# Kernel tuning notes

Measured on AMD Instinct MI355X. Metric: run time of the kernel, lower is better.

Reference implementation:

```python
import jax, jax.numpy as jnp
import numpy as np

SAMPLE = 16          # init kwarg `sample`
DILATED_RATE = 2     # init kwarg `dilated_rate`
RADIUS = 16.0        # hardcoded in forward: ball_query(16, ...)
NSAMPLE = SAMPLE * DILATED_RATE
XYZ_SCALE = 30.0     # spread points so radius-16 ball is a real neighborhood


def setup_inputs() -> dict:
    key = jax.random.key(0)
    k1, k2 = jax.random.split(key)
    xyz = jax.random.normal(k1, (4, 4096, 3), dtype=jnp.float32) * XYZ_SCALE
    feature = jax.random.normal(k2, (4, 4096, 64), dtype=jnp.float32)
    return {"xyz": xyz, "feature": feature}


def _ball_query(xyz, radius, nsample):
    """pointnet2-style ball query: for each point, the first `nsample` point
    indices (in ascending index order) with squared distance < radius^2;
    rows with fewer than nsample hits are padded with the first hit.
    xyz: [B,N,3] -> idx int32 [B,N,nsample]."""
    B, N, _ = xyz.shape
    sq = jnp.sum(xyz * xyz, axis=-1)                                   # [B,N]
    d2 = sq[:, :, None] + sq[:, None, :] - 2.0 * jnp.einsum(
        'bnd,bmd->bnm', xyz, xyz)                                      # [B,N,N]
    in_ball = d2 < (radius * radius)
    # score = N - j for in-ball points, 0 otherwise; top_k then returns the
    # smallest in-ball indices j, already sorted ascending in j.
    col_score = (N - jnp.arange(N, dtype=jnp.int32))[None, None, :]
    score = jnp.where(in_ball, col_score, 0)                           # [B,N,N]
    vals, idx = jax.lax.top_k(score, nsample)                          # [B,N,K]
    first = idx[..., 0:1]
    return jnp.where(vals > 0, idx, first)                             # pad with first hit


def _group(points, idx):
    """grouping_operation: points [B,N,C] (channel-last), idx [B,N,K] ->
    grouped [B,C,N,K]."""
    gathered = jax.vmap(lambda p, i: p[i])(points, idx)  # [B,N,K,C]
    return gathered.transpose(0, 3, 1, 2)                # [B,C,N,K]


def reference(xyz, feature):
    ids = _ball_query(xyz, RADIUS, NSAMPLE)              # [B,N,NSAMPLE]
    center = ids[:, :, 0:1]
    if DILATED_RATE == 1:
        dilated_ids = ids[:, :, :SAMPLE]
    else:
        region = ids[:, :, (DILATED_RATE - 1) * SAMPLE: DILATED_RATE * SAMPLE - 1]
        dilated_ids = jnp.concatenate([center, region], axis=-1)  # [B,N,SAMPLE]
    dilated_xyz = _group(xyz, dilated_ids)          # [B,3,N,SAMPLE]
    dilated_feature = _group(feature, dilated_ids)  # [B,C,N,SAMPLE]
    return (dilated_xyz, dilated_feature)
```

## Files before the change

### kernel.cpp

```cpp
#include <hip/hip_runtime.h>


#define BB 4
#define NN 4096
#define KK 16
#define PLANE (NN * KK)
#define NC 20
#define NCELLS (NC * NC * NC)

__device__ __forceinline__ int cell1d(float v)
{
    int c = (int)floorf((v + 160.0f) * 0.0625f);
    c = c < 0 ? 0 : c;
    return c > (NC - 1) ? (NC - 1) : c;
}

__global__ __launch_bounds__(256)
void preprocess(const float* __restrict__ xyz, float4* __restrict__ P,
                float4* __restrict__ SP, int* __restrict__ CS)
{
#pragma clang fp contract(off)
    __shared__ int hist[NCELLS];
    __shared__ int wsum[4];

    const int b = blockIdx.x;
    const int t = threadIdx.x;
    const int lane = t & 63, wave = t >> 6;
    const float* xb = xyz + b * NN * 3;

    for (int c = t; c < NCELLS; c += 256) hist[c] = 0;
    __syncthreads();

    for (int i = t; i < NN; i += 256) {
        const float x = xb[3 * i], y = xb[3 * i + 1], z = xb[3 * i + 2];
        const float sq = (x * x + y * y) + z * z;
        P[(b << 12) + i] = make_float4(x, y, z, sq);
        const int c = (cell1d(z) * NC + cell1d(y)) * NC + cell1d(x);
        atomicAdd(&hist[c], 1);
    }
    __syncthreads();

    const int c0 = t * 32;
    const int c1 = (c0 + 32 < NCELLS) ? c0 + 32 : NCELLS;
    int s = 0;
    for (int c = c0; c < c1; ++c) s += hist[c];
    int x = s;
#pragma unroll
    for (int off = 1; off < 64; off <<= 1) {
        const int u = __shfl_up(x, off, 64);
        if (lane >= off) x += u;
    }
    if (lane == 63) wsum[wave] = x;
    __syncthreads();
    int wb = 0;
    for (int w = 0; w < wave; ++w) wb += wsum[w];
    int acc = wb + x - s;

    int* cs = CS + b * (NCELLS + 1);
    for (int c = c0; c < c1; ++c) {
        const int v = hist[c];
        cs[c]   = acc;
        hist[c] = acc;
        acc += v;
    }
    if (t == 0) cs[NCELLS] = NN;
    __syncthreads();

    for (int i = t; i < NN; i += 256) {
        const float x = xb[3 * i], y = xb[3 * i + 1], z = xb[3 * i + 2];
        const int c = (cell1d(z) * NC + cell1d(y)) * NC + cell1d(x);
        const int slot = atomicAdd(&hist[c], 1);
        SP[(b << 12) + slot] = make_float4(x, y, z, __int_as_float(i));
    }
}

__global__ __launch_bounds__(256, 4)
void query_gather(const float4* __restrict__ P, const float4* __restrict__ SP,
                  const int* __restrict__ CS, const float* __restrict__ feat,
                  float* __restrict__ out)
{
#pragma clang fp contract(off)
    __shared__ unsigned int mask[4][128];
    __shared__ int sids[4 * KK];

    const int beta = blockIdx.x;
    const int b    = beta >> 10;
    const int p0   = (beta & 1023) * 4;
    const int t    = threadIdx.x;
    const int lane = t & 63;
    const int wave = t >> 6;

    ((unsigned int*)mask)[t]       = 0u;
    ((unsigned int*)mask)[t + 256] = 0u;
    __syncthreads();

    const float4* Pb  = P  + (b << 12);
    const float4* Sb  = SP + (b << 12);
    const int*    csb = CS + b * (NCELLS + 1);

    const float4 pi = Pb[p0 + wave];

    {
        const float sqi = pi.w;
        unsigned int* m = mask[wave];
        const int cx = cell1d(pi.x), cy = cell1d(pi.y), cz = cell1d(pi.z);
        const int xlo = cx > 0 ? cx - 1 : 0;
        const int xhi = cx < NC - 1 ? cx + 1 : NC - 1;

        int ss[9], se[9];
#pragma unroll
        for (int dz = 0; dz < 3; ++dz)
#pragma unroll
            for (int dy = 0; dy < 3; ++dy) {
                int zz = cz + dz - 1; zz = zz < 0 ? 0 : (zz > NC - 1 ? NC - 1 : zz);
                int yy = cy + dy - 1; yy = yy < 0 ? 0 : (yy > NC - 1 ? NC - 1 : yy);
                const int cb = (zz * NC + yy) * NC;
                ss[dz * 3 + dy] = csb[cb + xlo];
                se[dz * 3 + dy] = csb[cb + xhi + 1];
            }

        int off[10], base[9];
        off[0] = 0;
#pragma unroll
        for (int i = 0; i < 9; ++i) {
            off[i + 1] = off[i] + (se[i] - ss[i]);
            base[i]    = ss[i] - off[i];
        }
        const int T = off[9];

        for (int u = lane; u < T; u += 64) {
            int bsel = base[0];
#pragma unroll
            for (int i = 1; i < 9; ++i) bsel = (u >= off[i]) ? base[i] : bsel;
            const float4 a = Sb[u + bsel];
            const float sqj = (a.x * a.x + a.y * a.y) + a.z * a.z;
            const float dot = (pi.x * a.x + pi.y * a.y) + pi.z * a.z;
            const float d2  = (sqi + sqj) - 2.0f * dot;
            if (d2 < 256.0f) {
                const int j = __float_as_int(a.w);
                atomicOr(&m[j >> 5], 1u << (j & 31));
            }
        }
    }
    __syncthreads();

    {
        const unsigned int* m = mask[wave];
        const unsigned int lo  = m[2 * lane];
        const unsigned int hiw = m[2 * lane + 1];
        const unsigned long long w = ((unsigned long long)hiw << 32) | lo;
        const int c = __popcll(w);
        int x = c;
#pragma unroll
        for (int off = 1; off < 64; off <<= 1) {
            const int u = __shfl_up(x, off, 64);
            if (lane >= off) x += u;
        }
        const int cnt  = __shfl(x, 63, 64);
        const int base = x - c;

        int fj = 0x7fffffff;
        if (w) fj = (lane << 6) + __builtin_ctzll(w);
        for (int off = 32; off; off >>= 1) {
            const int o = __shfl_xor(fj, off, 64);
            fj = fj < o ? fj : o;
        }

        int* row = sids + wave * KK;
        if (w && base <= 30 && base + c > 16) {
            unsigned long long ww = w;
            int r = base;
            while (ww) {
                if (r > 30) break;
                if (r >= 16) row[r - 15] = (lane << 6) + __builtin_ctzll(ww);
                ww &= ww - 1;
                ++r;
            }
        }
        const int hi = (cnt < 31 ? cnt : 31) - 16;
        if (lane < KK && (lane == 0 || lane > hi)) row[lane] = fj;
    }
    __syncthreads();

    const int rowi = t & 63;
    const int part = t >> 6;
    const int id   = sids[rowi];
    const int ob   = (beta & 1023) * 64 + rowi;

    if (part == 0) {
        const float4 p = Pb[id];
        float* o0 = out + (size_t)b * 3 * PLANE + ob;
        o0[0]         = p.x;
        o0[PLANE]     = p.y;
        o0[2 * PLANE] = p.z;
    }

    const float4* frow = reinterpret_cast<const float4*>(feat + ((size_t)(b << 12) + id) * 64) + part * 4;
    float* o1 = out + (size_t)BB * 3 * PLANE + (size_t)b * 64 * PLANE
                    + (size_t)(part * 16) * PLANE + ob;
#pragma unroll
    for (int q = 0; q < 4; ++q) {
        const float4 v = frow[q];
        float* oc = o1 + (size_t)(4 * q) * PLANE;
        oc[0]         = v.x;
        oc[PLANE]     = v.y;
        oc[2 * PLANE] = v.z;
        oc[3 * PLANE] = v.w;
    }
}

extern "C" void kernel_launch(void* const* d_in, const int* in_sizes, int n_in,
                              void* d_out, int out_size, void* d_ws, size_t ws_size,
                              hipStream_t stream) {
    const float* xyz  = (const float*)d_in[0];
    const float* feat = (const float*)d_in[1];
    float* out = (float*)d_out;

    char* ws = (char*)d_ws;
    float4* P         = (float4*)(ws);
    float4* SP        = (float4*)(ws + 262144);
    int*    CS        = (int*)   (ws + 524288);

    preprocess  <<<BB,           256, 0, stream>>>(xyz, P, SP, CS);
    query_gather<<<BB * NN / 4,  256, 0, stream>>>(P, SP, CS, feat, out);
}
```

Before: 115.4 us.

## Process queries in cell-sorted order, prefetch candidates, and pad histogram to cut conflicts

Each block now takes its four query points from the cell-sorted array rather than in original index order. Neighbouring blocks therefore scan overlapping cells, which should improve cache reuse of candidate points. The output offset is recovered from the stored original index. The candidate loop is software-pipelined so the next chunk's load is issued before the current chunk's distance test. Each wave clears and uses its own mask, which lets the block-wide barriers around the scan be dropped. The preprocess histogram is padded every 32 entries to reduce LDS bank conflicts. The risks are scattered output writes, since consecutive blocks no longer write contiguous rows, and reliance on wave-level ordering of LDS operations now that the barriers are gone.

```diff
diff --git a/kernel.cpp b/kernel.cpp
--- a/kernel.cpp
+++ b/kernel.cpp
@@ -7,6 +7,7 @@
 #define PLANE (NN * KK)
 #define NC 20
 #define NCELLS (NC * NC * NC)
+#define HP(c) ((c) + ((c) >> 5))
 
 __device__ __forceinline__ int cell1d(float v)
 {
@@ -20,7 +21,7 @@
                 float4* __restrict__ SP, int* __restrict__ CS)
 {
 #pragma clang fp contract(off)
-    __shared__ int hist[NCELLS];
+    __shared__ int hist[HP(NCELLS - 1) + 1 + 8];
     __shared__ int wsum[4];
 
     const int b = blockIdx.x;
@@ -28,7 +29,7 @@
     const int lane = t & 63, wave = t >> 6;
     const float* xb = xyz + b * NN * 3;
 
-    for (int c = t; c < NCELLS; c += 256) hist[c] = 0;
+    for (int c = t; c < NCELLS; c += 256) hist[HP(c)] = 0;
     __syncthreads();
 
     for (int i = t; i < NN; i += 256) {
@@ -36,14 +37,14 @@
         const float sq = (x * x + y * y) + z * z;
         P[(b << 12) + i] = make_float4(x, y, z, sq);
         const int c = (cell1d(z) * NC + cell1d(y)) * NC + cell1d(x);
-        atomicAdd(&hist[c], 1);
+        atomicAdd(&hist[HP(c)], 1);
     }
     __syncthreads();
 
     const int c0 = t * 32;
     const int c1 = (c0 + 32 < NCELLS) ? c0 + 32 : NCELLS;
     int s = 0;
-    for (int c = c0; c < c1; ++c) s += hist[c];
+    for (int c = c0; c < c1; ++c) s += hist[HP(c)];
     int x = s;
 #pragma unroll
     for (int off = 1; off < 64; off <<= 1) {
@@ -58,9 +59,9 @@
 
     int* cs = CS + b * (NCELLS + 1);
     for (int c = c0; c < c1; ++c) {
-        const int v = hist[c];
-        cs[c]   = acc;
-        hist[c] = acc;
+        const int v = hist[HP(c)];
+        cs[c]      = acc;
+        hist[HP(c)] = acc;
         acc += v;
     }
     if (t == 0) cs[NCELLS] = NN;
@@ -69,7 +70,7 @@
     for (int i = t; i < NN; i += 256) {
         const float x = xb[3 * i], y = xb[3 * i + 1], z = xb[3 * i + 2];
         const int c = (cell1d(z) * NC + cell1d(y)) * NC + cell1d(x);
-        const int slot = atomicAdd(&hist[c], 1);
+        const int slot = atomicAdd(&hist[HP(c)], 1);
         SP[(b << 12) + slot] = make_float4(x, y, z, __int_as_float(i));
     }
 }
@@ -82,28 +83,29 @@
 #pragma clang fp contract(off)
     __shared__ unsigned int mask[4][128];
     __shared__ int sids[4 * KK];
+    __shared__ int jof[4];
 
     const int beta = blockIdx.x;
     const int b    = beta >> 10;
-    const int p0   = (beta & 1023) * 4;
+    const int q0   = (beta & 1023) * 4;
     const int t    = threadIdx.x;
     const int lane = t & 63;
     const int wave = t >> 6;
 
-    ((unsigned int*)mask)[t]       = 0u;
-    ((unsigned int*)mask)[t + 256] = 0u;
-    __syncthreads();
-
     const float4* Pb  = P  + (b << 12);
     const float4* Sb  = SP + (b << 12);
     const int*    csb = CS + b * (NCELLS + 1);
 
-    const float4 pi = Pb[p0 + wave];
+    const float4 pr  = Sb[q0 + wave];
+    const float  sqi = (pr.x * pr.x + pr.y * pr.y) + pr.z * pr.z;
+    if (lane == 0) jof[wave] = __float_as_int(pr.w);
+
+    unsigned int* m = mask[wave];
+    m[2 * lane]     = 0u;
+    m[2 * lane + 1] = 0u;
 
     {
-        const float sqi = pi.w;
-        unsigned int* m = mask[wave];
-        const int cx = cell1d(pi.x), cy = cell1d(pi.y), cz = cell1d(pi.z);
+        const int cx = cell1d(pr.x), cy = cell1d(pr.y), cz = cell1d(pr.z);
         const int xlo = cx > 0 ? cx - 1 : 0;
         const int xhi = cx < NC - 1 ? cx + 1 : NC - 1;
 
@@ -128,24 +130,33 @@
         }
         const int T = off[9];
 
-        for (int u = lane; u < T; u += 64) {
-            int bsel = base[0];
-#pragma unroll
-            for (int i = 1; i < 9; ++i) bsel = (u >= off[i]) ? base[i] : bsel;
-            const float4 a = Sb[u + bsel];
+        auto sbaddr = [&](int u) {
+            int bs = base[0];
+#pragma unroll
+            for (int i = 1; i < 9; ++i) bs = (u >= off[i]) ? base[i] : bs;
+            return u + bs;
+        };
+
+        const int nch = (T + 63) >> 6;
+        float4 a = Sb[sbaddr(lane < T ? lane : T - 1)];
+        for (int c = 0; c < nch; ++c) {
+            float4 nx;
+            if (c + 1 < nch) {
+                const int un0 = lane + ((c + 1) << 6);
+                nx = Sb[sbaddr(un0 < T ? un0 : T - 1)];
+            }
             const float sqj = (a.x * a.x + a.y * a.y) + a.z * a.z;
-            const float dot = (pi.x * a.x + pi.y * a.y) + pi.z * a.z;
+            const float dot = (pr.x * a.x + pr.y * a.y) + pr.z * a.z;
             const float d2  = (sqi + sqj) - 2.0f * dot;
             if (d2 < 256.0f) {
                 const int j = __float_as_int(a.w);
                 atomicOr(&m[j >> 5], 1u << (j & 31));
             }
-        }
-    }
-    __syncthreads();
+            a = nx;
+        }
+    }
 
     {
-        const unsigned int* m = mask[wave];
         const unsigned int lo  = m[2 * lane];
         const unsigned int hiw = m[2 * lane + 1];
         const unsigned long long w = ((unsigned long long)hiw << 32) | lo;
@@ -185,7 +196,7 @@
     const int rowi = t & 63;
     const int part = t >> 6;
     const int id   = sids[rowi];
-    const int ob   = (beta & 1023) * 64 + rowi;
+    const int ob   = jof[rowi >> 4] * KK + (rowi & 15);
 
     if (part == 0) {
         const float4 p = Pb[id];
@@ -217,10 +228,10 @@
     float* out = (float*)d_out;
 
     char* ws = (char*)d_ws;
-    float4* P         = (float4*)(ws);
-    float4* SP        = (float4*)(ws + 262144);
-    int*    CS        = (int*)   (ws + 524288);
-
-    preprocess  <<<BB,           256, 0, stream>>>(xyz, P, SP, CS);
-    query_gather<<<BB * NN / 4,  256, 0, stream>>>(P, SP, CS, feat, out);
-}
+    float4* P  = (float4*)(ws);
+    float4* SP = (float4*)(ws + 262144);
+    int*    CS = (int*)   (ws + 524288);
+
+    preprocess  <<<BB,          256, 0, stream>>>(xyz, P, SP, CS);
+    query_gather<<<BB * NN / 4, 256, 0, stream>>>(P, SP, CS, feat, out);
+}
```

New measurement: 125.2 us. +8.5%, slower.

## Switch 3D cell grid to 2D xy columns and drop block-wide syncs

Applied to the files above, without the earlier changes.

The spatial grid now bins points only by x and y (20x20 columns) instead of a 20x20x20 voxel grid. The query therefore scans three contiguous column ranges, which removes the per-candidate 9-way segment selection. The per-wave mask is now cleared by its own wave, so the two __syncthreads around the candidate scan are dropped and only a wave-local dependency remains. The trade is more candidates per query, since the full z extent is scanned. Correctness also relies on wave-level LDS ordering without an explicit barrier.

```diff
diff --git a/kernel.cpp b/kernel.cpp
--- a/kernel.cpp
+++ b/kernel.cpp
@@ -6,7 +6,7 @@
 #define KK 16
 #define PLANE (NN * KK)
 #define NC 20
-#define NCELLS (NC * NC * NC)
+#define NCELL2 (NC * NC)
 
 __device__ __forceinline__ int cell1d(float v)
 {
@@ -20,7 +20,7 @@
                 float4* __restrict__ SP, int* __restrict__ CS)
 {
 #pragma clang fp contract(off)
-    __shared__ int hist[NCELLS];
+    __shared__ int hist[NCELL2];
     __shared__ int wsum[4];
 
     const int b = blockIdx.x;
@@ -28,20 +28,21 @@
     const int lane = t & 63, wave = t >> 6;
     const float* xb = xyz + b * NN * 3;
 
-    for (int c = t; c < NCELLS; c += 256) hist[c] = 0;
+    if (t < NCELL2) hist[t] = 0;
+    if (t + 256 < NCELL2) hist[t + 256] = 0;
     __syncthreads();
 
     for (int i = t; i < NN; i += 256) {
         const float x = xb[3 * i], y = xb[3 * i + 1], z = xb[3 * i + 2];
         const float sq = (x * x + y * y) + z * z;
         P[(b << 12) + i] = make_float4(x, y, z, sq);
-        const int c = (cell1d(z) * NC + cell1d(y)) * NC + cell1d(x);
+        const int c = cell1d(y) * NC + cell1d(x);
         atomicAdd(&hist[c], 1);
     }
     __syncthreads();
 
-    const int c0 = t * 32;
-    const int c1 = (c0 + 32 < NCELLS) ? c0 + 32 : NCELLS;
+    const int c0 = t * 2;
+    const int c1 = (c0 + 2 < NCELL2) ? c0 + 2 : NCELL2;
     int s = 0;
     for (int c = c0; c < c1; ++c) s += hist[c];
     int x = s;
@@ -56,19 +57,19 @@
     for (int w = 0; w < wave; ++w) wb += wsum[w];
     int acc = wb + x - s;
 
-    int* cs = CS + b * (NCELLS + 1);
+    int* cs = CS + b * (NCELL2 + 1);
     for (int c = c0; c < c1; ++c) {
         const int v = hist[c];
         cs[c]   = acc;
         hist[c] = acc;
         acc += v;
     }
-    if (t == 0) cs[NCELLS] = NN;
+    if (t == 0) cs[NCELL2] = NN;
     __syncthreads();
 
     for (int i = t; i < NN; i += 256) {
         const float x = xb[3 * i], y = xb[3 * i + 1], z = xb[3 * i + 2];
-        const int c = (cell1d(z) * NC + cell1d(y)) * NC + cell1d(x);
+        const int c = cell1d(y) * NC + cell1d(x);
         const int slot = atomicAdd(&hist[c], 1);
         SP[(b << 12) + slot] = make_float4(x, y, z, __int_as_float(i));
     }
@@ -90,62 +91,42 @@
     const int lane = t & 63;
     const int wave = t >> 6;
 
-    ((unsigned int*)mask)[t]       = 0u;
-    ((unsigned int*)mask)[t + 256] = 0u;
-    __syncthreads();
-
     const float4* Pb  = P  + (b << 12);
     const float4* Sb  = SP + (b << 12);
-    const int*    csb = CS + b * (NCELLS + 1);
-
-    const float4 pi = Pb[p0 + wave];
+    const int*    csb = CS + b * (NCELL2 + 1);
+
+    const float4 pi  = Pb[p0 + wave];
+    const float  sqi = pi.w;
+
+    unsigned int* m = mask[wave];
+    m[2 * lane]     = 0u;
+    m[2 * lane + 1] = 0u;
 
     {
-        const float sqi = pi.w;
-        unsigned int* m = mask[wave];
-        const int cx = cell1d(pi.x), cy = cell1d(pi.y), cz = cell1d(pi.z);
+        const int cx = cell1d(pi.x), cy = cell1d(pi.y);
         const int xlo = cx > 0 ? cx - 1 : 0;
         const int xhi = cx < NC - 1 ? cx + 1 : NC - 1;
-
-        int ss[9], se[9];
-#pragma unroll
-        for (int dz = 0; dz < 3; ++dz)
-#pragma unroll
-            for (int dy = 0; dy < 3; ++dy) {
-                int zz = cz + dz - 1; zz = zz < 0 ? 0 : (zz > NC - 1 ? NC - 1 : zz);
-                int yy = cy + dy - 1; yy = yy < 0 ? 0 : (yy > NC - 1 ? NC - 1 : yy);
-                const int cb = (zz * NC + yy) * NC;
-                ss[dz * 3 + dy] = csb[cb + xlo];
-                se[dz * 3 + dy] = csb[cb + xhi + 1];
+#pragma unroll
+        for (int rr = 0; rr < 3; ++rr) {
+            int yy = cy + rr - 1;
+            yy = yy < 0 ? 0 : (yy > NC - 1 ? NC - 1 : yy);
+            const int cb = yy * NC;
+            const int s  = csb[cb + xlo];
+            const int e  = csb[cb + xhi + 1];
+            for (int v = s + lane; v < e; v += 64) {
+                const float4 a = Sb[v];
+                const float sqj = (a.x * a.x + a.y * a.y) + a.z * a.z;
+                const float dot = (pi.x * a.x + pi.y * a.y) + pi.z * a.z;
+                const float d2  = (sqi + sqj) - 2.0f * dot;
+                if (d2 < 256.0f) {
+                    const int j = __float_as_int(a.w);
+                    atomicOr(&m[j >> 5], 1u << (j & 31));
+                }
             }
-
-        int off[10], base[9];
-        off[0] = 0;
-#pragma unroll
-        for (int i = 0; i < 9; ++i) {
-            off[i + 1] = off[i] + (se[i] - ss[i]);
-            base[i]    = ss[i] - off[i];
-        }
-        const int T = off[9];
-
-        for (int u = lane; u < T; u += 64) {
-            int bsel = base[0];
-#pragma unroll
-            for (int i = 1; i < 9; ++i) bsel = (u >= off[i]) ? base[i] : bsel;
-            const float4 a = Sb[u + bsel];
-            const float sqj = (a.x * a.x + a.y * a.y) + a.z * a.z;
-            const float dot = (pi.x * a.x + pi.y * a.y) + pi.z * a.z;
-            const float d2  = (sqi + sqj) - 2.0f * dot;
-            if (d2 < 256.0f) {
-                const int j = __float_as_int(a.w);
-                atomicOr(&m[j >> 5], 1u << (j & 31));
-            }
-        }
-    }
-    __syncthreads();
+        }
+    }
 
     {
-        const unsigned int* m = mask[wave];
         const unsigned int lo  = m[2 * lane];
         const unsigned int hiw = m[2 * lane + 1];
         const unsigned long long w = ((unsigned long long)hiw << 32) | lo;
@@ -217,10 +198,10 @@
     float* out = (float*)d_out;
 
     char* ws = (char*)d_ws;
-    float4* P         = (float4*)(ws);
-    float4* SP        = (float4*)(ws + 262144);
-    int*    CS        = (int*)   (ws + 524288);
-
-    preprocess  <<<BB,           256, 0, stream>>>(xyz, P, SP, CS);
-    query_gather<<<BB * NN / 4,  256, 0, stream>>>(P, SP, CS, feat, out);
-}
+    float4* P  = (float4*)(ws);
+    float4* SP = (float4*)(ws + 262144);
+    int*    CS = (int*)   (ws + 524288);
+
+    preprocess  <<<BB,          256, 0, stream>>>(xyz, P, SP, CS);
+    query_gather<<<BB * NN / 4, 256, 0, stream>>>(P, SP, CS, feat, out);
+}
```

After: 114.1 us. No clear change (-1.1%).
